# Optimization experiments

Measured on AMD Instinct MI355X. Metric: run time of the kernel, lower is better.

## Reference

```python
import jax, jax.numpy as jnp
import numpy as np

B, NQ, NK = 2, 2048, 2048
QD, CD, H, DH = 1024, 768, 16, 64
INNER = H * DH


def setup_inputs() -> dict:
    key = jax.random.key(0)
    ks = jax.random.split(key, 8)
    x = jax.random.normal(ks[0], (B, NQ, QD), jnp.float32)
    context = jax.random.normal(ks[1], (B, NK, CD), jnp.float32)
    mask = jax.random.randint(ks[2], (B, 1, NQ, NK), 0, 2) > 0
    s = lambda d: 1.0 / np.sqrt(d)
    Wq = jax.random.normal(ks[3], (INNER, QD), jnp.float32) * s(QD)
    Wk = jax.random.normal(ks[4], (INNER, CD), jnp.float32) * s(CD)
    Wv = jax.random.normal(ks[5], (INNER, CD), jnp.float32) * s(CD)
    Wo = jax.random.normal(ks[6], (QD, INNER), jnp.float32) * s(INNER)
    bo = jax.random.normal(ks[7], (QD,), jnp.float32) * 0.01
    return {"x": x, "context": context, "mask": mask,
            "Wq": Wq, "Wk": Wk, "Wv": Wv, "Wo": Wo, "bo": bo}


def reference(x, context, mask, Wq, Wk, Wv, Wo, bo):
    scale = DH ** -0.5
    # QKV projections (Linear, no bias): [b, n, inner] -> [b, n, h, d]
    q = (x @ Wq.T).reshape(B, NQ, H, DH)
    k = (context @ Wk.T).reshape(B, NK, H, DH)
    v = (context @ Wv.T).reshape(B, NK, H, DH)
    # additive bias built from boolean mask (masked_fill with -finfo.max/2)
    max_neg = -jnp.finfo(q.dtype).max / 2
    bias = jnp.where(mask, jnp.zeros((), q.dtype), max_neg)  # [b,1,nq,nk]
    scores = jnp.einsum('bqhd,bkhd->bhqk', q, k) * scale + bias
    attn = jax.nn.softmax(scores, axis=-1)
    out = jnp.einsum('bhqk,bkhd->bqhd', attn, v).reshape(B, NQ, INNER)
    return out @ Wo.T + bo
```

## Files before the change

kernel.cpp:

```cpp
#include <hip/hip_runtime.h>
#include <float.h>
#include <stdint.h>

#define C_B     2
#define C_NQ    2048
#define C_NK    2048
#define C_QD    1024
#define C_CD    768
#define C_H     16
#define C_DH    64
#define C_INNER 1024

typedef __bf16 bf16;
typedef __attribute__((ext_vector_type(8))) __bf16 bf16x8;
typedef __attribute__((ext_vector_type(4))) __bf16 bf16x4;
typedef __attribute__((ext_vector_type(4))) float f32x4;
typedef __attribute__((ext_vector_type(16))) float f32x16;

#if __has_builtin(__builtin_amdgcn_exp2f)
#define EXP2(x) __builtin_amdgcn_exp2f(x)
#else
#define EXP2(x) __expf((x) * 0.69314718056f)
#endif

__device__ __forceinline__ void async_copy16(const bf16* g, bf16* l) {
  __builtin_amdgcn_global_load_lds(
      (const __attribute__((address_space(1))) void*)g,
      (__attribute__((address_space(3))) void*)l,
      16, 0, 0);
}

__global__ __launch_bounds__(256) void cvt_all(const float* __restrict__ s0, const float* __restrict__ s1,
                                               const float* __restrict__ s2, const float* __restrict__ s3,
                                               const float* __restrict__ s4, const float* __restrict__ s5,
                                               bf16* __restrict__ d0, bf16* __restrict__ d1,
                                               bf16* __restrict__ d2, bf16* __restrict__ d3,
                                               bf16* __restrict__ d4, bf16* __restrict__ d5) {
  const int stride = gridDim.x * blockDim.x;
  for (int idx = blockIdx.x * blockDim.x + threadIdx.x; idx < 2752512; idx += stride) {
    const float* src; bf16* dst; int loc;
    if      (idx < 1048576) { src = s0; dst = d0; loc = idx; }
    else if (idx < 1835008) { src = s1; dst = d1; loc = idx - 1048576; }
    else if (idx < 2097152) { src = s2; dst = d2; loc = idx - 1835008; }
    else if (idx < 2293760) { src = s3; dst = d3; loc = idx - 2097152; }
    else if (idx < 2490368) { src = s4; dst = d4; loc = idx - 2293760; }
    else                    { src = s5; dst = d5; loc = idx - 2490368; }
    float4 f = *(const float4*)&src[loc * 4];
    bf16x4 o = { (bf16)f.x, (bf16)f.y, (bf16)f.z, (bf16)f.w };
    *(bf16x4*)&dst[loc * 4] = o;
  }
}

__global__ __launch_bounds__(256) void pack_mask(const int* __restrict__ mask,
                                                 unsigned long long* __restrict__ mb,
                                                 int nwords) {
  const int wid  = (blockIdx.x * blockDim.x + threadIdx.x) >> 6;
  const int lane = threadIdx.x & 63;
  const int nw   = (gridDim.x * blockDim.x) >> 6;
  for (int w = wid; w < nwords; w += nw) {
    int v = mask[(size_t)w * 64 + lane];
    unsigned long long bb = __ballot(v != 0);
    if (lane == 0) mb[w] = bb;
  }
}

template <int OUTBF16, int HASBIAS>
__global__ __launch_bounds__(256) void gemm_bt(const bf16* __restrict__ A,
                                               const bf16* __restrict__ W,
                                               const float* __restrict__ bias,
                                               void* __restrict__ Cout,
                                               int M, int N, int K, float oscale,
                                               int ncut, bf16* __restrict__ Cout2) {
  __shared__ __align__(16) bf16 As[2][128 * 32];
  __shared__ __align__(16) bf16 Bs[2][128 * 32];

  const int t = threadIdx.x;
  const int w = t >> 6, lane = t & 63;
  const int l15 = lane & 15, lg = lane >> 4;
  const int wm = w >> 1, wn = w & 1;
  const int m0 = blockIdx.y * 128, n0 = blockIdx.x * 128;

  f32x4 acc[4][4] = {};

  auto stage = [&](int nb, int k0) {
#pragma unroll
    for (int i = 0; i < 2; ++i) {
      const int chunk = w * 128 + i * 64 + lane;
      const int row = chunk >> 2;
      const int srcb = ((chunk & 3) ^ (row & 3)) * 8;
      async_copy16(A + (size_t)(m0 + row) * K + k0 + srcb, &As[nb][chunk * 8]);
      async_copy16(W + (size_t)(n0 + row) * K + k0 + srcb, &Bs[nb][chunk * 8]);
    }
  };

  stage(0, 0);
  int cur = 0;
  for (int k0 = 0; k0 < K; k0 += 32) {
    __syncthreads();
    if (k0 + 32 < K) stage(cur ^ 1, k0 + 32);

    bf16x8 af[4], bfv[4];
#pragma unroll
    for (int mi = 0; mi < 4; ++mi) {
      const int row = wm * 64 + mi * 16 + l15;
      af[mi] = *(const bf16x8*)&As[cur][row * 32 + ((lg ^ (row & 3)) * 8)];
    }
#pragma unroll
    for (int ni = 0; ni < 4; ++ni) {
      const int row = wn * 64 + ni * 16 + l15;
      bfv[ni] = *(const bf16x8*)&Bs[cur][row * 32 + ((lg ^ (row & 3)) * 8)];
    }
#pragma unroll
    for (int mi = 0; mi < 4; ++mi)
#pragma unroll
      for (int ni = 0; ni < 4; ++ni)
        acc[mi][ni] = __builtin_amdgcn_mfma_f32_16x16x32_bf16(af[mi], bfv[ni],
                                                              acc[mi][ni], 0, 0, 0);
    cur ^= 1;
  }

#pragma unroll
  for (int mi = 0; mi < 4; ++mi)
#pragma unroll
    for (int ni = 0; ni < 4; ++ni)
#pragma unroll
      for (int r = 0; r < 4; ++r) {
        const int row = m0 + wm * 64 + mi * 16 + lg * 4 + r;
        const int col = n0 + wn * 64 + ni * 16 + l15;
        float v = acc[mi][ni][r] * oscale;
        if (HASBIAS) v += bias[col];
        if (OUTBF16) {
          bf16* dst; int cc, str;
          if (col < ncut) { dst = (bf16*)Cout; cc = col; str = ncut; }
          else            { dst = Cout2; cc = col - ncut; str = N - ncut; }
          dst[(size_t)row * str + cc] = (bf16)v;
        } else {
          ((float*)Cout)[(size_t)row * N + col] = v;
        }
      }
}

__global__ __launch_bounds__(256) void vtrans(const bf16* __restrict__ V,
                                              bf16* __restrict__ Vt) {
  __shared__ __align__(16) bf16 T[64][80];
  const int kt = blockIdx.x, h = blockIdx.y, b = blockIdx.z;
  const int t = threadIdx.x;
  {
    const int kl = t >> 2, db = (t & 3) * 16;
    const bf16* src = &V[((size_t)(b * C_NK + kt * 64 + kl)) * C_INNER + h * 64 + db];
    *(bf16x8*)&T[kl][db]     = *(const bf16x8*)&src[0];
    *(bf16x8*)&T[kl][db + 8] = *(const bf16x8*)&src[8];
  }
  __syncthreads();
  {
    const int d = t >> 2, kb = (t & 3) * 16;
    const int P0[8] = {0, 1, 2, 3, 8, 9, 10, 11};
    const int P1[8] = {4, 5, 6, 7, 12, 13, 14, 15};
    bf16x8 o0, o1;
#pragma unroll
    for (int j = 0; j < 8; ++j) { o0[j] = T[kb + P0[j]][d]; o1[j] = T[kb + P1[j]][d]; }
    bf16* dst = &Vt[((size_t)((b * C_H + h) * C_DH + d)) * C_NK + kt * 64 + kb];
    *(bf16x8*)&dst[0] = o0;
    *(bf16x8*)&dst[8] = o1;
  }
}

__global__ __launch_bounds__(256, 4) void attn_fwd(const bf16* __restrict__ Q,
                                                   const bf16* __restrict__ K,
                                                   const bf16* __restrict__ Vt,
                                                   const unsigned long long* __restrict__ MB,
                                                   bf16* __restrict__ O0,
                                                   bf16* __restrict__ O1,
                                                   float2* __restrict__ LM) {
  __shared__ __align__(16) bf16 Ks[2][64 * 64];
  __shared__ __align__(16) bf16 Vs[2][64 * 64];

  const int qt = blockIdx.x, h = blockIdx.y;
  const int half = blockIdx.z >> 1, b = blockIdx.z & 1;
  const int t = threadIdx.x, wq = t >> 6, lane = t & 63;
  const int l31 = lane & 31, hi = lane >> 5;
  const int q = qt * 128 + wq * 32 + l31;

  bf16x8 qf[4];
  {
    const bf16* qp = Q + ((size_t)(b * C_NQ + q)) * C_INNER + h * C_DH;
#pragma unroll
    for (int db = 0; db < 4; ++db)
      qf[db] = *(const bf16x8*)&qp[db * 16 + hi * 8];
  }

  float m_run = -3.0e38f, l_run = 0.f;
  f32x16 acc_o[2] = {};

  auto stage = [&](int nb, int ktA) {
#pragma unroll
    for (int i = 0; i < 2; ++i) {
      const int chunk = wq * 128 + i * 64 + lane;
      const int row = chunk >> 3, pcb = chunk & 7;
      const int srcb = (pcb ^ (row & 7)) * 8;
      const bf16* kg = K + ((size_t)(b * C_NK + ktA * 64 + row)) * C_INNER + h * C_DH + srcb;
      async_copy16(kg, &Ks[nb][chunk * 8]);
      const bf16* vg = Vt + ((size_t)((b * C_H + h) * C_DH + row)) * C_NK + ktA * 64 + srcb;
      async_copy16(vg, &Vs[nb][chunk * 8]);
    }
  };

  const int kt0 = half * 16;
  stage(0, kt0);
  int cur = 0;

  for (int i = 0; i < 16; ++i) {
    const int ktA = kt0 + i;
    const unsigned long long wd =
        MB[((size_t)(b * C_NQ + q)) * (C_NK / 64) + ktA] >> (hi * 4);
    const unsigned mlo = (unsigned)wd, mhi = (unsigned)(wd >> 32);

    __syncthreads();
    if (i + 1 < 16) stage(cur ^ 1, ktA + 1);

    f32x16 s[2] = {};
    __builtin_amdgcn_s_setprio(1);
#pragma unroll
    for (int kb = 0; kb < 2; ++kb)
#pragma unroll
      for (int db = 0; db < 4; ++db) {
        const int row = kb * 32 + l31;
        const int cb = (db * 2 + hi) ^ (row & 7);
        bf16x8 kf = *(const bf16x8*)&Ks[cur][row * 64 + cb * 8];
        s[kb] = __builtin_amdgcn_mfma_f32_32x32x16_bf16(kf, qf[db], s[kb], 0, 0, 0);
      }
    __builtin_amdgcn_s_setprio(0);

    float pm = -1.0e30f;
#pragma unroll
    for (int kb = 0; kb < 2; ++kb)
#pragma unroll
      for (int reg = 0; reg < 16; ++reg) pm = fmaxf(pm, s[kb][reg]);
    pm = fmaxf(pm, __shfl_xor(pm, 32));

    if (!__all(pm <= m_run + 8.0f)) {
      const float mn = fmaxf(m_run, pm);
      const float f = EXP2(m_run - mn);
      m_run = mn;
      l_run *= f;
#pragma unroll
      for (int d2 = 0; d2 < 2; ++d2)
#pragma unroll
        for (int reg = 0; reg < 16; ++reg)
          acc_o[d2][reg] *= f;
    }

    bf16x8 pfr[4];
    float ps = 0.f;
#pragma unroll
    for (int kb = 0; kb < 2; ++kb) {
      const unsigned mw = kb ? mhi : mlo;
#pragma unroll
      for (int kss = 0; kss < 2; ++kss) {
        bf16x8 pf;
#pragma unroll
        for (int j = 0; j < 8; ++j) {
          const int reg = kss * 8 + j;
          const int pos = (reg & 3) + 8 * (reg >> 2);
          float p = EXP2(s[kb][reg] - m_run);
          p = ((mw >> pos) & 1u) ? p : 0.f;
          ps += p;
          pf[j] = (bf16)p;
        }
        pfr[kb * 2 + kss] = pf;
      }
    }
    l_run += ps;

    __builtin_amdgcn_s_setprio(1);
#pragma unroll
    for (int ks = 0; ks < 4; ++ks) {
#pragma unroll
      for (int d2 = 0; d2 < 2; ++d2) {
        const int row = d2 * 32 + l31;
        const int cb = (ks * 2 + hi) ^ (row & 7);
        bf16x8 vf = *(const bf16x8*)&Vs[cur][row * 64 + cb * 8];
        acc_o[d2] = __builtin_amdgcn_mfma_f32_32x32x16_bf16(vf, pfr[ks], acc_o[d2], 0, 0, 0);
      }
    }
    __builtin_amdgcn_s_setprio(0);
    cur ^= 1;
  }

  {
    const float l_tot = l_run + __shfl_xor(l_run, 32);
    const size_t row = (size_t)(b * C_H + h) * C_NQ + q;
    bf16* op = (half ? O1 : O0) + row * 64;
#pragma unroll
    for (int d2 = 0; d2 < 2; ++d2)
#pragma unroll
      for (int bb = 0; bb < 4; ++bb) {
        bf16x4 o;
#pragma unroll
        for (int rr = 0; rr < 4; ++rr)
          o[rr] = (bf16)(acc_o[d2][bb * 4 + rr]);
        *(bf16x4*)&op[d2 * 32 + bb * 8 + hi * 4] = o;
      }
    if (hi == 0) LM[(size_t)half * 65536 + row] = make_float2(m_run, l_tot);
  }
}

__global__ __launch_bounds__(256) void merge_halves(const bf16* __restrict__ O0,
                                                    const bf16* __restrict__ O1,
                                                    const float2* __restrict__ LM,
                                                    bf16* __restrict__ AO) {
  const int t = threadIdx.x;
  const int r = blockIdx.x * 32 + (t >> 3);
  const int dc = (t & 7) * 8;
  const float2 lm0 = LM[r], lm1 = LM[65536 + r];
  const float ms = fmaxf(lm0.x, lm1.x);
  const float w0 = EXP2(lm0.x - ms), w1 = EXP2(lm1.x - ms);
  const float denom = lm0.y * w0 + lm1.y * w1;
  const float s0 = w0 / denom, s1 = w1 / denom;
  bf16x8 a = *(const bf16x8*)&O0[(size_t)r * 64 + dc];
  bf16x8 c = *(const bf16x8*)&O1[(size_t)r * 64 + dc];
  bf16x8 o;
#pragma unroll
  for (int j = 0; j < 8; ++j)
    o[j] = (bf16)((float)a[j] * s0 + (float)c[j] * s1);
  const int q = r & 2047, bh = r >> 11, hh = bh & 15, bb = bh >> 4;
  *(bf16x8*)&AO[((size_t)(bb * C_NQ + q)) * C_INNER + hh * 64 + dc] = o;
}

extern "C" void kernel_launch(void* const* d_in, const int* in_sizes, int n_in,
                              void* d_out, int out_size, void* d_ws, size_t ws_size,
                              hipStream_t stream) {
  const float* x   = (const float*)d_in[0];
  const float* ctx = (const float*)d_in[1];
  const int*   msk = (const int*)d_in[2];
  const float* Wq  = (const float*)d_in[3];
  const float* Wk  = (const float*)d_in[4];
  const float* Wv  = (const float*)d_in[5];
  const float* Wo  = (const float*)d_in[6];
  const float* bo  = (const float*)d_in[7];
  float* out = (float*)d_out;

  bf16* ws  = (bf16*)d_ws;
  bf16* xb  = ws;
  bf16* cb  = xb  + 4194304;
  bf16* wqb = cb  + 3145728;
  bf16* wkb = wqb + 1048576;
  bf16* wvb = wkb + 786432;
  bf16* wob = wvb + 786432;
  bf16* Qb  = wob + 1048576;
  bf16* Kb  = Qb  + 4194304;
  bf16* Vb  = Kb  + 4194304;
  bf16* AOb = Vb  + 4194304;
  unsigned long long* mb = (unsigned long long*)(AOb + 4194304);
  float2* lm = (float2*)(mb + 131072);
  bf16* Vtb = xb;
  bf16* O0  = cb;
  bf16* O1  = Vb;

  dim3 blk(256);
  cvt_all<<<2048, blk, 0, stream>>>(x, ctx, Wq, Wk, Wv, Wo, xb, cb, wqb, wkb, wvb, wob);

  pack_mask<<<512, blk, 0, stream>>>(msk, mb, C_B * C_NQ * (C_NK / 64));

  const int MQ = C_B * C_NQ;
  const float qscale = 0.125f * 1.44269504f;
  gemm_bt<1, 0><<<dim3(C_INNER / 128, MQ / 128), blk, 0, stream>>>(
      xb, wqb, nullptr, Qb, MQ, C_INNER, C_QD, qscale, C_INNER, nullptr);
  gemm_bt<1, 0><<<dim3(2 * C_INNER / 128, MQ / 128), blk, 0, stream>>>(
      cb, wkb, nullptr, Kb, MQ, 2 * C_INNER, C_CD, 1.0f, C_INNER, Vb);

  vtrans<<<dim3(C_NK / 64, C_H, C_B), blk, 0, stream>>>(Vb, Vtb);

  attn_fwd<<<dim3(C_NQ / 128, C_H, 2 * C_B), blk, 0, stream>>>(
      Qb, Kb, Vtb, mb, O0, O1, lm);

  merge_halves<<<2048, blk, 0, stream>>>(O0, O1, lm, AOb);

  gemm_bt<0, 1><<<dim3(C_QD / 128, MQ / 128), blk, 0, stream>>>(
      AOb, wob, bo, out, MQ, C_QD, C_INNER, 1.0f, C_QD, nullptr);
}
```

Before: 173.4 us.

## Merge prep and QKV GEMM launches, swizzle attention block order

Folds the mask-packing kernel into the fp32-to-bf16 conversion kernel and runs the Q and KV projection GEMMs as one 768-block launch. This cuts kernel launches and lets the tail of one GEMM overlap the other. The attention kernel moves to a 1D grid with a swizzled block index that interleaves heads, batches and halves across consecutive blocks, aiming for better cache locality and load balance. The added branching in the QKV epilogue and the loss of the template specialisation add a little per-thread overhead.

```diff
diff --git a/kernel.cpp b/kernel.cpp
--- a/kernel.cpp
+++ b/kernel.cpp
@@ -30,12 +30,14 @@
       16, 0, 0);
 }
 
-__global__ __launch_bounds__(256) void cvt_all(const float* __restrict__ s0, const float* __restrict__ s1,
-                                               const float* __restrict__ s2, const float* __restrict__ s3,
-                                               const float* __restrict__ s4, const float* __restrict__ s5,
-                                               bf16* __restrict__ d0, bf16* __restrict__ d1,
-                                               bf16* __restrict__ d2, bf16* __restrict__ d3,
-                                               bf16* __restrict__ d4, bf16* __restrict__ d5) {
+__global__ __launch_bounds__(256) void prep(const float* __restrict__ s0, const float* __restrict__ s1,
+                                            const float* __restrict__ s2, const float* __restrict__ s3,
+                                            const float* __restrict__ s4, const float* __restrict__ s5,
+                                            bf16* __restrict__ d0, bf16* __restrict__ d1,
+                                            bf16* __restrict__ d2, bf16* __restrict__ d3,
+                                            bf16* __restrict__ d4, bf16* __restrict__ d5,
+                                            const int* __restrict__ mask,
+                                            unsigned long long* __restrict__ mb) {
   const int stride = gridDim.x * blockDim.x;
   for (int idx = blockIdx.x * blockDim.x + threadIdx.x; idx < 2752512; idx += stride) {
     const float* src; bf16* dst; int loc;
@@ -49,38 +51,26 @@
     bf16x4 o = { (bf16)f.x, (bf16)f.y, (bf16)f.z, (bf16)f.w };
     *(bf16x4*)&dst[loc * 4] = o;
   }
-}
-
-__global__ __launch_bounds__(256) void pack_mask(const int* __restrict__ mask,
-                                                 unsigned long long* __restrict__ mb,
-                                                 int nwords) {
+  const int lane = threadIdx.x & 63;
   const int wid  = (blockIdx.x * blockDim.x + threadIdx.x) >> 6;
-  const int lane = threadIdx.x & 63;
   const int nw   = (gridDim.x * blockDim.x) >> 6;
-  for (int w = wid; w < nwords; w += nw) {
+  for (int w = wid; w < 131072; w += nw) {
     int v = mask[(size_t)w * 64 + lane];
     unsigned long long bb = __ballot(v != 0);
     if (lane == 0) mb[w] = bb;
   }
 }
 
-template <int OUTBF16, int HASBIAS>
-__global__ __launch_bounds__(256) void gemm_bt(const bf16* __restrict__ A,
-                                               const bf16* __restrict__ W,
-                                               const float* __restrict__ bias,
-                                               void* __restrict__ Cout,
-                                               int M, int N, int K, float oscale,
-                                               int ncut, bf16* __restrict__ Cout2) {
-  __shared__ __align__(16) bf16 As[2][128 * 32];
-  __shared__ __align__(16) bf16 Bs[2][128 * 32];
-
-  const int t = threadIdx.x;
-  const int w = t >> 6, lane = t & 63;
+__device__ __forceinline__ void gemm_core(const bf16* __restrict__ A,
+                                          const bf16* __restrict__ W,
+                                          int m0, int n0, int K,
+                                          bf16* As0, bf16* As1, bf16* Bs0, bf16* Bs1,
+                                          f32x4 (&acc)[4][4],
+                                          int w, int lane) {
   const int l15 = lane & 15, lg = lane >> 4;
   const int wm = w >> 1, wn = w & 1;
-  const int m0 = blockIdx.y * 128, n0 = blockIdx.x * 128;
-
-  f32x4 acc[4][4] = {};
+  bf16* AsA[2] = {As0, As1};
+  bf16* BsA[2] = {Bs0, Bs1};
 
   auto stage = [&](int nb, int k0) {
 #pragma unroll
@@ -88,8 +78,8 @@
       const int chunk = w * 128 + i * 64 + lane;
       const int row = chunk >> 2;
       const int srcb = ((chunk & 3) ^ (row & 3)) * 8;
-      async_copy16(A + (size_t)(m0 + row) * K + k0 + srcb, &As[nb][chunk * 8]);
-      async_copy16(W + (size_t)(n0 + row) * K + k0 + srcb, &Bs[nb][chunk * 8]);
+      async_copy16(A + (size_t)(m0 + row) * K + k0 + srcb, &AsA[nb][chunk * 8]);
+      async_copy16(W + (size_t)(n0 + row) * K + k0 + srcb, &BsA[nb][chunk * 8]);
     }
   };
 
@@ -103,12 +93,12 @@
 #pragma unroll
     for (int mi = 0; mi < 4; ++mi) {
       const int row = wm * 64 + mi * 16 + l15;
-      af[mi] = *(const bf16x8*)&As[cur][row * 32 + ((lg ^ (row & 3)) * 8)];
+      af[mi] = *(const bf16x8*)&AsA[cur][row * 32 + ((lg ^ (row & 3)) * 8)];
     }
 #pragma unroll
     for (int ni = 0; ni < 4; ++ni) {
       const int row = wn * 64 + ni * 16 + l15;
-      bfv[ni] = *(const bf16x8*)&Bs[cur][row * 32 + ((lg ^ (row & 3)) * 8)];
+      bfv[ni] = *(const bf16x8*)&BsA[cur][row * 32 + ((lg ^ (row & 3)) * 8)];
     }
 #pragma unroll
     for (int mi = 0; mi < 4; ++mi)
@@ -118,6 +108,38 @@
                                                               acc[mi][ni], 0, 0, 0);
     cur ^= 1;
   }
+}
+
+__global__ __launch_bounds__(256) void gemm_qkv(const bf16* __restrict__ xb,
+                                                const bf16* __restrict__ wqb,
+                                                bf16* __restrict__ Qb,
+                                                const bf16* __restrict__ cb,
+                                                const bf16* __restrict__ wkv,
+                                                bf16* __restrict__ Kb,
+                                                bf16* __restrict__ Vb,
+                                                float qscale) {
+  __shared__ __align__(16) bf16 As[2][128 * 32];
+  __shared__ __align__(16) bf16 Bs[2][128 * 32];
+
+  const int bid = blockIdx.x;
+  const int t = threadIdx.x, w = t >> 6, lane = t & 63;
+  const int l15 = lane & 15, lg = lane >> 4;
+  const int wm = w >> 1, wn = w & 1;
+
+  const bf16 *A, *W;
+  int m0, n0, K, N;
+  float oscale;
+  if (bid < 256) {
+    A = xb; W = wqb; n0 = (bid & 7) * 128; m0 = (bid >> 3) * 128;
+    K = C_QD; N = C_INNER; oscale = qscale;
+  } else {
+    const int b2 = bid - 256;
+    A = cb; W = wkv; n0 = (b2 & 15) * 128; m0 = (b2 >> 4) * 128;
+    K = C_CD; N = 2 * C_INNER; oscale = 1.0f;
+  }
+
+  f32x4 acc[4][4] = {};
+  gemm_core(A, W, m0, n0, K, As[0], As[1], Bs[0], Bs[1], acc, w, lane);
 
 #pragma unroll
   for (int mi = 0; mi < 4; ++mi)
@@ -127,16 +149,39 @@
       for (int r = 0; r < 4; ++r) {
         const int row = m0 + wm * 64 + mi * 16 + lg * 4 + r;
         const int col = n0 + wn * 64 + ni * 16 + l15;
-        float v = acc[mi][ni][r] * oscale;
-        if (HASBIAS) v += bias[col];
-        if (OUTBF16) {
-          bf16* dst; int cc, str;
-          if (col < ncut) { dst = (bf16*)Cout; cc = col; str = ncut; }
-          else            { dst = Cout2; cc = col - ncut; str = N - ncut; }
-          dst[(size_t)row * str + cc] = (bf16)v;
-        } else {
-          ((float*)Cout)[(size_t)row * N + col] = v;
-        }
+        const float v = acc[mi][ni][r] * oscale;
+        bf16* dst; int cc;
+        if (bid < 256)            { dst = Qb; cc = col; }
+        else if (col < C_INNER)   { dst = Kb; cc = col; }
+        else                      { dst = Vb; cc = col - C_INNER; }
+        dst[(size_t)row * C_INNER + cc] = (bf16)v;
+      }
+}
+
+__global__ __launch_bounds__(256) void gemm_out(const bf16* __restrict__ A,
+                                                const bf16* __restrict__ W,
+                                                const float* __restrict__ bias,
+                                                float* __restrict__ Cout,
+                                                int M, int N, int K) {
+  __shared__ __align__(16) bf16 As[2][128 * 32];
+  __shared__ __align__(16) bf16 Bs[2][128 * 32];
+  const int t = threadIdx.x, w = t >> 6, lane = t & 63;
+  const int l15 = lane & 15, lg = lane >> 4;
+  const int wm = w >> 1, wn = w & 1;
+  const int m0 = blockIdx.y * 128, n0 = blockIdx.x * 128;
+
+  f32x4 acc[4][4] = {};
+  gemm_core(A, W, m0, n0, K, As[0], As[1], Bs[0], Bs[1], acc, w, lane);
+
+#pragma unroll
+  for (int mi = 0; mi < 4; ++mi)
+#pragma unroll
+    for (int ni = 0; ni < 4; ++ni)
+#pragma unroll
+      for (int r = 0; r < 4; ++r) {
+        const int row = m0 + wm * 64 + mi * 16 + lg * 4 + r;
+        const int col = n0 + wn * 64 + ni * 16 + l15;
+        Cout[(size_t)row * N + col] = acc[mi][ni][r] + bias[col];
       }
 }
 
@@ -175,8 +220,10 @@
   __shared__ __align__(16) bf16 Ks[2][64 * 64];
   __shared__ __align__(16) bf16 Vs[2][64 * 64];
 
-  const int qt = blockIdx.x, h = blockIdx.y;
-  const int half = blockIdx.z >> 1, b = blockIdx.z & 1;
+  const int bid = blockIdx.x;
+  const int swz = ((bid & 7) << 7) | (bid >> 3);
+  const int qt = swz & 15, h = (swz >> 4) & 15, zz = swz >> 8;
+  const int half = zz >> 1, b = zz & 1;
   const int t = threadIdx.x, wq = t >> 6, lane = t & 63;
   const int l31 = lane & 31, hi = lane >> 5;
   const int q = qt * 128 + wq * 32 + l31;
@@ -358,24 +405,19 @@
   bf16* O1  = Vb;
 
   dim3 blk(256);
-  cvt_all<<<2048, blk, 0, stream>>>(x, ctx, Wq, Wk, Wv, Wo, xb, cb, wqb, wkb, wvb, wob);
-
-  pack_mask<<<512, blk, 0, stream>>>(msk, mb, C_B * C_NQ * (C_NK / 64));
+  prep<<<2048, blk, 0, stream>>>(x, ctx, Wq, Wk, Wv, Wo,
+                                 xb, cb, wqb, wkb, wvb, wob, msk, mb);
+
+  const float qscale = 0.125f * 1.44269504f;
+  gemm_qkv<<<768, blk, 0, stream>>>(xb, wqb, Qb, cb, wkb, Kb, Vb, qscale);
+
+  vtrans<<<dim3(C_NK / 64, C_H, C_B), blk, 0, stream>>>(Vb, Vtb);
+
+  attn_fwd<<<1024, blk, 0, stream>>>(Qb, Kb, Vtb, mb, O0, O1, lm);
+
+  merge_halves<<<2048, blk, 0, stream>>>(O0, O1, lm, AOb);
 
   const int MQ = C_B * C_NQ;
-  const float qscale = 0.125f * 1.44269504f;
-  gemm_bt<1, 0><<<dim3(C_INNER / 128, MQ / 128), blk, 0, stream>>>(
-      xb, wqb, nullptr, Qb, MQ, C_INNER, C_QD, qscale, C_INNER, nullptr);
-  gemm_bt<1, 0><<<dim3(2 * C_INNER / 128, MQ / 128), blk, 0, stream>>>(
-      cb, wkb, nullptr, Kb, MQ, 2 * C_INNER, C_CD, 1.0f, C_INNER, Vb);
-
-  vtrans<<<dim3(C_NK / 64, C_H, C_B), blk, 0, stream>>>(Vb, Vtb);
-
-  attn_fwd<<<dim3(C_NQ / 128, C_H, 2 * C_B), blk, 0, stream>>>(
-      Qb, Kb, Vtb, mb, O0, O1, lm);
-
-  merge_halves<<<2048, blk, 0, stream>>>(O0, O1, lm, AOb);
-
-  gemm_bt<0, 1><<<dim3(C_QD / 128, MQ / 128), blk, 0, stream>>>(
-      AOb, wob, bo, out, MQ, C_QD, C_INNER, 1.0f, C_QD, nullptr);
-}
+  gemm_out<<<dim3(C_QD / 128, MQ / 128), blk, 0, stream>>>(
+      AOb, wob, bo, out, MQ, C_QD, C_INNER);
+}
```

Result: faster. 153.0 us (-11.8%).
